# Optimization experiments

Measured on AMD Instinct MI355X. Metric: run time of the kernel, lower is better.

The kernel has to match this reference:

```python
import jax, jax.numpy as jnp
import numpy as np

DILATIONS = [1, 2, 4, 8, 16, 32, 64, 128, 256, 1, 2, 4, 8, 16, 32, 64, 128, 256]
KSIZE = 3
CHAN = 16
NUM_SIG = 1       # num_channels in original
NUM_CTRL = 3      # control channels appended to signal
FRAME_SIZE = 2048
R = sum(d * (KSIZE - 1) for d in DILATIONS) + 1  # 2045
BATCH = 64
T = FRAME_SIZE + R - 1  # 4092


def causal_conv1d(x, w, b, dil):
    # x: [B,T,Cin], w: [K,Cin,Cout] (Keras layout), causal left pad dil*(K-1)
    pad = dil * (w.shape[0] - 1)
    y = jax.lax.conv_general_dilated(
        x, w, window_strides=(1,), padding=[(pad, 0)],
        rhs_dilation=(dil,), dimension_numbers=("NWC", "WIO", "NWC"))
    return y + b


def setup_inputs() -> dict:
    key = jax.random.key(0)
    ks = jax.random.split(key, 8)
    n_layers = len(DILATIONS)
    in0 = NUM_SIG + NUM_CTRL            # layer 0 sees 1 signal + 3 controls = 4
    in_rest = CHAN + NUM_CTRL           # layers 1.. see 16-ch signal + 3 controls = 19
    s = 0.1
    inp = {
        "input": jax.random.normal(ks[0], (BATCH, T, in0), dtype=jnp.float32),
        "conv_w0": jax.random.normal(ks[1], (KSIZE, in0, CHAN), dtype=jnp.float32) * s,
        "conv_w": jax.random.normal(ks[2], (n_layers - 1, KSIZE, in_rest, CHAN), dtype=jnp.float32) * s,
        "conv_b": jax.random.normal(ks[3], (n_layers, CHAN), dtype=jnp.float32) * s,
        "io_w": jax.random.normal(ks[4], (n_layers - 1, CHAN, CHAN), dtype=jnp.float32) * s,
        "io_b": jax.random.normal(ks[5], (n_layers - 1, CHAN), dtype=jnp.float32) * s,
        "mixer_w": jax.random.normal(ks[6], (n_layers * CHAN, NUM_SIG), dtype=jnp.float32) * s,
        "mixer_b": jax.random.normal(ks[7], (NUM_SIG,), dtype=jnp.float32) * s,
    }
    return inp


def reference(input, conv_w0, conv_w, conv_b, io_w, io_b, mixer_w, mixer_b):
    signal = input[:, :, :NUM_SIG]        # [B,T,1]
    controls = input[:, :, NUM_SIG:]      # [B,T,3]
    n_layers = len(DILATIONS)
    acc = []
    for i in range(n_layers):
        w = conv_w0 if i == 0 else conv_w[i - 1]
        h = jnp.concatenate([signal, controls], axis=2)
        h = causal_conv1d(h, w, conv_b[i], DILATIONS[i])
        h = jax.nn.relu(h)                # [B,T,16]
        acc.append(h)
        if i != n_layers - 1:
            # 1x1 conv residual mix + halved channel-sum skip of previous signal
            signal = (jnp.einsum("btc,co->bto", h, io_w[i]) + io_b[i]
                      + jnp.sum(signal, axis=2, keepdims=True) / 2)
    accumulator = jnp.concatenate(acc, axis=2)  # [B,T,288]
    mixed = jnp.einsum("btc,co->bto", accumulator, mixer_w) + mixer_b
    return mixed[:, -FRAME_SIZE:, :]
```

## Files before the change

### kernel.cpp

```cpp
#include <hip/hip_runtime.h>

#define TFULL 4092
#define NB    64
#define CH    16
#define OUT_T 2048
#define TOFF  2044

__global__ __launch_bounds__(256) void layer0_kernel(
    const float* __restrict__ input,
    const float* __restrict__ w,
    const float* __restrict__ bias,
    const float* __restrict__ iow,
    const float* __restrict__ iob,
    const float* __restrict__ mw,
    const float* __restrict__ mb,
    float* __restrict__ sig_out,
    float* __restrict__ out)
{
    const int b = blockIdx.y;
    const int t = blockIdx.x * 256 + threadIdx.x;
    if (t >= TFULL) return;
    const float* ib = input + ((size_t)b * TFULL) * 4;

    float h[CH];
    #pragma unroll
    for (int o = 0; o < CH; ++o) h[o] = bias[o];

    float sig_t = 0.f;
    #pragma unroll
    for (int k = 0; k < 3; ++k) {
        const int tt = t - (2 - k);
        if (tt >= 0) {
            const float4 x = *(const float4*)(ib + (size_t)tt * 4);
            if (k == 2) sig_t = x.x;
            const float xv[4] = {x.x, x.y, x.z, x.w};
            #pragma unroll
            for (int c = 0; c < 4; ++c) {
                const float v = xv[c];
                #pragma unroll
                for (int o = 0; o < CH; ++o)
                    h[o] = fmaf(v, w[(k * 4 + c) * CH + o], h[o]);
            }
        }
    }
    #pragma unroll
    for (int o = 0; o < CH; ++o) h[o] = fmaxf(h[o], 0.f);

    if (t >= TOFF) {
        float m = mb[0];
        #pragma unroll
        for (int o = 0; o < CH; ++o) m = fmaf(h[o], mw[o], m);
        out[(size_t)b * OUT_T + (t - TOFF)] = m;
    }

    float sn[CH];
    const float half = sig_t * 0.5f;
    #pragma unroll
    for (int o = 0; o < CH; ++o) sn[o] = iob[o] + half;
    #pragma unroll
    for (int c = 0; c < CH; ++c) {
        const float v = h[c];
        #pragma unroll
        for (int o = 0; o < CH; ++o)
            sn[o] = fmaf(v, iow[c * CH + o], sn[o]);
    }
    float* op = sig_out + ((size_t)b * TFULL + t) * CH;
    *(float4*)(op + 0)  = make_float4(sn[0],  sn[1],  sn[2],  sn[3]);
    *(float4*)(op + 4)  = make_float4(sn[4],  sn[5],  sn[6],  sn[7]);
    *(float4*)(op + 8)  = make_float4(sn[8],  sn[9],  sn[10], sn[11]);
    *(float4*)(op + 12) = make_float4(sn[12], sn[13], sn[14], sn[15]);
}

template <bool HAS_IO>
__global__ __launch_bounds__(256) void layer_kernel(
    const float* __restrict__ input,
    const float* __restrict__ sig_in,
    const float* __restrict__ w,
    const float* __restrict__ bias,
    const float* __restrict__ iow,
    const float* __restrict__ iob,
    const float* __restrict__ mw,
    float* __restrict__ sig_out,
    float* __restrict__ out,
    int dil, int t_start)
{
    const int b = blockIdx.y;
    const int t = t_start + blockIdx.x * 256 + threadIdx.x;
    if (t >= TFULL) return;
    const float* ib = input  + ((size_t)b * TFULL) * 4;
    const float* sb = sig_in + ((size_t)b * TFULL) * CH;

    float h[CH];
    #pragma unroll
    for (int o = 0; o < CH; ++o) h[o] = bias[o];

    float sum_t = 0.f;
    #pragma unroll
    for (int k = 0; k < 3; ++k) {
        const int tt = t - (2 - k) * dil;
        if (tt >= 0) {
            const float4* sp = (const float4*)(sb + (size_t)tt * CH);
            const float4 s0 = sp[0], s1 = sp[1], s2 = sp[2], s3 = sp[3];
            const float sv[CH] = {s0.x, s0.y, s0.z, s0.w, s1.x, s1.y, s1.z, s1.w,
                                  s2.x, s2.y, s2.z, s2.w, s3.x, s3.y, s3.z, s3.w};
            const float4 cc = *(const float4*)(ib + (size_t)tt * 4);
            if (k == 2) {
                float acc = 0.f;
                #pragma unroll
                for (int c = 0; c < CH; ++c) acc += sv[c];
                sum_t = acc;
            }
            #pragma unroll
            for (int c = 0; c < CH; ++c) {
                const float v = sv[c];
                #pragma unroll
                for (int o = 0; o < CH; ++o)
                    h[o] = fmaf(v, w[(k * 19 + c) * CH + o], h[o]);
            }
            const float cv[3] = {cc.y, cc.z, cc.w};
            #pragma unroll
            for (int c = 0; c < 3; ++c) {
                const float v = cv[c];
                #pragma unroll
                for (int o = 0; o < CH; ++o)
                    h[o] = fmaf(v, w[(k * 19 + 16 + c) * CH + o], h[o]);
            }
        }
    }
    #pragma unroll
    for (int o = 0; o < CH; ++o) h[o] = fmaxf(h[o], 0.f);

    if (t >= TOFF) {
        float m = 0.f;
        #pragma unroll
        for (int o = 0; o < CH; ++o) m = fmaf(h[o], mw[o], m);
        const size_t oi = (size_t)b * OUT_T + (t - TOFF);
        out[oi] += m;
    }

    if (HAS_IO) {
        float sn[CH];
        const float half = sum_t * 0.5f;
        #pragma unroll
        for (int o = 0; o < CH; ++o) sn[o] = iob[o] + half;
        #pragma unroll
        for (int c = 0; c < CH; ++c) {
            const float v = h[c];
            #pragma unroll
            for (int o = 0; o < CH; ++o)
                sn[o] = fmaf(v, iow[c * CH + o], sn[o]);
        }
        float* op = sig_out + ((size_t)b * TFULL + t) * CH;
        *(float4*)(op + 0)  = make_float4(sn[0],  sn[1],  sn[2],  sn[3]);
        *(float4*)(op + 4)  = make_float4(sn[4],  sn[5],  sn[6],  sn[7]);
        *(float4*)(op + 8)  = make_float4(sn[8],  sn[9],  sn[10], sn[11]);
        *(float4*)(op + 12) = make_float4(sn[12], sn[13], sn[14], sn[15]);
    }
}

extern "C" void kernel_launch(void* const* d_in, const int* in_sizes, int n_in,
                              void* d_out, int out_size, void* d_ws, size_t ws_size,
                              hipStream_t stream) {
    const float* input   = (const float*)d_in[0];
    const float* conv_w0 = (const float*)d_in[1];
    const float* conv_w  = (const float*)d_in[2];
    const float* conv_b  = (const float*)d_in[3];
    const float* io_w    = (const float*)d_in[4];
    const float* io_b    = (const float*)d_in[5];
    const float* mixer_w = (const float*)d_in[6];
    const float* mixer_b = (const float*)d_in[7];
    float* out = (float*)d_out;

    float* sigA = (float*)d_ws;
    float* sigB = sigA + (size_t)NB * TFULL * CH;

    static const int dil[18] = {1,2,4,8,16,32,64,128,256, 1,2,4,8,16,32,64,128,256};
    static const int ts[18]  = {0,2,6,14,30,62,126,254,510,
                                1022,1024,1028,1036,1052,1084,1148,1276,1532};
    static const int ts17 = 2044;

    {
        dim3 grid((TFULL + 255) / 256, NB);
        layer0_kernel<<<grid, 256, 0, stream>>>(input, conv_w0, conv_b, io_w, io_b,
                                                mixer_w, mixer_b, sigA, out);
    }
    const float* cur = sigA;
    float* nxt = sigB;
    for (int i = 1; i < 18; ++i) {
        const int t0 = (i == 17) ? ts17 : ts[i];
        const int len = TFULL - t0;
        dim3 grid((len + 255) / 256, NB);
        const float* wl = conv_w + (size_t)(i - 1) * 3 * 19 * 16;
        if (i < 17) {
            layer_kernel<true><<<grid, 256, 0, stream>>>(
                input, cur, wl, conv_b + i * CH,
                io_w + (size_t)i * CH * CH, io_b + (size_t)i * CH,
                mixer_w + i * CH, nxt, out, dil[i], t0);
        } else {
            layer_kernel<false><<<grid, 256, 0, stream>>>(
                input, cur, wl, conv_b + i * CH,
                nullptr, nullptr,
                mixer_w + i * CH, nullptr, out, dil[i], t0);
        }
        float* tmp = (float*)cur; cur = nxt; nxt = tmp;
    }
}
```

Baseline: 323.8 us.

## Fuse dilated conv layers into three grouped kernels with shared-memory halo tiles

```diff
diff --git a/kernel.cpp b/kernel.cpp
--- a/kernel.cpp
+++ b/kernel.cpp
@@ -5,156 +5,179 @@
 #define CH    16
 #define OUT_T 2048
 #define TOFF  2044
-
-__global__ __launch_bounds__(256) void layer0_kernel(
+#define NT    512
+#define RSTRIDE 20
+
+template<int L0, int NL, int TILE, int HALO, bool FIRSTG, bool LASTG>
+__global__ __launch_bounds__(NT, 2) void group_kernel(
     const float* __restrict__ input,
-    const float* __restrict__ w,
-    const float* __restrict__ bias,
-    const float* __restrict__ iow,
-    const float* __restrict__ iob,
-    const float* __restrict__ mw,
-    const float* __restrict__ mb,
+    const float* __restrict__ conv_w0,
+    const float* __restrict__ conv_w,
+    const float* __restrict__ conv_b,
+    const float* __restrict__ io_w,
+    const float* __restrict__ io_b,
+    const float* __restrict__ mixer_w,
+    const float* __restrict__ mixer_b,
+    const float* __restrict__ sig_in,
     float* __restrict__ sig_out,
-    float* __restrict__ out)
+    float* __restrict__ out,
+    int out_start)
 {
-    const int b = blockIdx.y;
-    const int t = blockIdx.x * 256 + threadIdx.x;
-    if (t >= TFULL) return;
-    const float* ib = input + ((size_t)b * TFULL) * 4;
-
-    float h[CH];
-    #pragma unroll
-    for (int o = 0; o < CH; ++o) h[o] = bias[o];
-
-    float sig_t = 0.f;
-    #pragma unroll
-    for (int k = 0; k < 3; ++k) {
-        const int tt = t - (2 - k);
-        if (tt >= 0) {
-            const float4 x = *(const float4*)(ib + (size_t)tt * 4);
-            if (k == 2) sig_t = x.x;
-            const float xv[4] = {x.x, x.y, x.z, x.w};
-            #pragma unroll
-            for (int c = 0; c < 4; ++c) {
-                const float v = xv[c];
-                #pragma unroll
-                for (int o = 0; o < CH; ++o)
-                    h[o] = fmaf(v, w[(k * 4 + c) * CH + o], h[o]);
+    constexpr int NROWS = TILE + HALO;
+    __shared__ float buf[NROWS * RSTRIDE];
+    __shared__ float macc[TILE];
+
+    const int b       = blockIdx.y;
+    const int tile_lo = out_start + blockIdx.x * TILE;
+    const int tile_hi = (tile_lo + TILE < TFULL) ? (tile_lo + TILE) : TFULL;
+    const int buf_lo  = tile_lo - HALO;
+    const int tid     = threadIdx.x;
+
+    {
+        const float* ib = input + ((size_t)b * TFULL + buf_lo) * 4;
+        const int nstage = tile_hi - buf_lo;
+        for (int j = tid; j < nstage; j += NT) {
+            *(float4*)(&buf[j * RSTRIDE + 16]) = *(const float4*)(ib + (size_t)j * 4);
+            if constexpr (!FIRSTG) {
+                const float* sp = sig_in + ((size_t)b * TFULL + (buf_lo + j)) * CH;
+                *(float4*)(&buf[j * RSTRIDE + 0])  = *(const float4*)(sp + 0);
+                *(float4*)(&buf[j * RSTRIDE + 4])  = *(const float4*)(sp + 4);
+                *(float4*)(&buf[j * RSTRIDE + 8])  = *(const float4*)(sp + 8);
+                *(float4*)(&buf[j * RSTRIDE + 12]) = *(const float4*)(sp + 12);
             }
         }
+        for (int j = tid; j < TILE; j += NT) macc[j] = 0.f;
     }
-    #pragma unroll
-    for (int o = 0; o < CH; ++o) h[o] = fmaxf(h[o], 0.f);
-
-    if (t >= TOFF) {
-        float m = mb[0];
-        #pragma unroll
-        for (int o = 0; o < CH; ++o) m = fmaf(h[o], mw[o], m);
-        out[(size_t)b * OUT_T + (t - TOFF)] = m;
-    }
-
-    float sn[CH];
-    const float half = sig_t * 0.5f;
-    #pragma unroll
-    for (int o = 0; o < CH; ++o) sn[o] = iob[o] + half;
-    #pragma unroll
-    for (int c = 0; c < CH; ++c) {
-        const float v = h[c];
-        #pragma unroll
-        for (int o = 0; o < CH; ++o)
-            sn[o] = fmaf(v, iow[c * CH + o], sn[o]);
-    }
-    float* op = sig_out + ((size_t)b * TFULL + t) * CH;
-    *(float4*)(op + 0)  = make_float4(sn[0],  sn[1],  sn[2],  sn[3]);
-    *(float4*)(op + 4)  = make_float4(sn[4],  sn[5],  sn[6],  sn[7]);
-    *(float4*)(op + 8)  = make_float4(sn[8],  sn[9],  sn[10], sn[11]);
-    *(float4*)(op + 12) = make_float4(sn[12], sn[13], sn[14], sn[15]);
-}
-
-template <bool HAS_IO>
-__global__ __launch_bounds__(256) void layer_kernel(
-    const float* __restrict__ input,
-    const float* __restrict__ sig_in,
-    const float* __restrict__ w,
-    const float* __restrict__ bias,
-    const float* __restrict__ iow,
-    const float* __restrict__ iob,
-    const float* __restrict__ mw,
-    float* __restrict__ sig_out,
-    float* __restrict__ out,
-    int dil, int t_start)
-{
-    const int b = blockIdx.y;
-    const int t = t_start + blockIdx.x * 256 + threadIdx.x;
-    if (t >= TFULL) return;
-    const float* ib = input  + ((size_t)b * TFULL) * 4;
-    const float* sb = sig_in + ((size_t)b * TFULL) * CH;
-
-    float h[CH];
-    #pragma unroll
-    for (int o = 0; o < CH; ++o) h[o] = bias[o];
-
-    float sum_t = 0.f;
-    #pragma unroll
-    for (int k = 0; k < 3; ++k) {
-        const int tt = t - (2 - k) * dil;
-        if (tt >= 0) {
-            const float4* sp = (const float4*)(sb + (size_t)tt * CH);
-            const float4 s0 = sp[0], s1 = sp[1], s2 = sp[2], s3 = sp[3];
-            const float sv[CH] = {s0.x, s0.y, s0.z, s0.w, s1.x, s1.y, s1.z, s1.w,
-                                  s2.x, s2.y, s2.z, s2.w, s3.x, s3.y, s3.z, s3.w};
-            const float4 cc = *(const float4*)(ib + (size_t)tt * 4);
-            if (k == 2) {
-                float acc = 0.f;
+    __syncthreads();
+
+    int lo = buf_lo;
+    for (int i = 0; i < NL; ++i) {
+        const int g   = L0 + i;
+        const int dil = 1 << (g % 9);
+        lo += 2 * dil;
+        const bool lastl = (i == NL - 1);
+        const float* wb   = (g == 0) ? conv_w0 : (conv_w + (size_t)(g - 1) * 3 * 19 * CH);
+        const float* bias = conv_b  + (size_t)g * CH;
+        const float* iw   = io_w    + (size_t)g * CH * CH;
+        const float* iob2 = io_b    + (size_t)g * CH;
+        const float* mw   = mixer_w + (size_t)g * CH;
+
+        const int n   = tile_hi - lo;
+        const int nch = (n + NT - 1) / NT;
+        for (int c = 0; c < nch; ++c) {
+            const int r   = tile_hi - (c + 1) * NT + tid;
+            const bool act = (r >= lo);
+            int j = 0;
+            float sn[CH];
+            if (act) {
+                j = r - buf_lo;
+                const float* r2 = &buf[j * RSTRIDE];
+                const float* r1 = &buf[(j - dil) * RSTRIDE];
+                const float* r0 = &buf[(j - 2 * dil) * RSTRIDE];
+
+                float h[CH];
                 #pragma unroll
-                for (int c = 0; c < CH; ++c) acc += sv[c];
-                sum_t = acc;
+                for (int o = 0; o < CH; ++o) h[o] = bias[o];
+                float sum_t;
+
+                if (FIRSTG && g == 0) {
+                    const float4 x0 = *(const float4*)(r0 + 16);
+                    const float4 x1 = *(const float4*)(r1 + 16);
+                    const float4 x2 = *(const float4*)(r2 + 16);
+                    const float t0[4] = {x0.x, x0.y, x0.z, x0.w};
+                    const float t1[4] = {x1.x, x1.y, x1.z, x1.w};
+                    const float t2[4] = {x2.x, x2.y, x2.z, x2.w};
+                    #pragma unroll
+                    for (int cc = 0; cc < 4; ++cc) {
+                        #pragma unroll
+                        for (int o = 0; o < CH; ++o) {
+                            h[o] = fmaf(t0[cc], wb[(0 * 4 + cc) * CH + o], h[o]);
+                            h[o] = fmaf(t1[cc], wb[(1 * 4 + cc) * CH + o], h[o]);
+                            h[o] = fmaf(t2[cc], wb[(2 * 4 + cc) * CH + o], h[o]);
+                        }
+                    }
+                    sum_t = x2.x;
+                } else {
+                    const float4 a0 = *(const float4*)(r0 + 0),  a1 = *(const float4*)(r0 + 4),
+                                 a2 = *(const float4*)(r0 + 8),  a3 = *(const float4*)(r0 + 12),
+                                 a4 = *(const float4*)(r0 + 16);
+                    const float4 b0 = *(const float4*)(r1 + 0),  b1 = *(const float4*)(r1 + 4),
+                                 b2 = *(const float4*)(r1 + 8),  b3 = *(const float4*)(r1 + 12),
+                                 b4 = *(const float4*)(r1 + 16);
+                    const float4 c0 = *(const float4*)(r2 + 0),  c1 = *(const float4*)(r2 + 4),
+                                 c2 = *(const float4*)(r2 + 8),  c3 = *(const float4*)(r2 + 12),
+                                 c4 = *(const float4*)(r2 + 16);
+                    const float t0[19] = {a0.x,a0.y,a0.z,a0.w, a1.x,a1.y,a1.z,a1.w,
+                                          a2.x,a2.y,a2.z,a2.w, a3.x,a3.y,a3.z,a3.w,
+                                          a4.y,a4.z,a4.w};
+                    const float t1[19] = {b0.x,b0.y,b0.z,b0.w, b1.x,b1.y,b1.z,b1.w,
+                                          b2.x,b2.y,b2.z,b2.w, b3.x,b3.y,b3.z,b3.w,
+                                          b4.y,b4.z,b4.w};
+                    const float t2[19] = {c0.x,c0.y,c0.z,c0.w, c1.x,c1.y,c1.z,c1.w,
+                                          c2.x,c2.y,c2.z,c2.w, c3.x,c3.y,c3.z,c3.w,
+                                          c4.y,c4.z,c4.w};
+                    #pragma unroll
+                    for (int cc = 0; cc < 19; ++cc) {
+                        #pragma unroll
+                        for (int o = 0; o < CH; ++o) {
+                            h[o] = fmaf(t0[cc], wb[(0 * 19 + cc) * CH + o], h[o]);
+                            h[o] = fmaf(t1[cc], wb[(1 * 19 + cc) * CH + o], h[o]);
+                            h[o] = fmaf(t2[cc], wb[(2 * 19 + cc) * CH + o], h[o]);
+                        }
+                    }
+                    sum_t = ((c0.x + c0.y) + (c0.z + c0.w)) + ((c1.x + c1.y) + (c1.z + c1.w))
+                          + ((c2.x + c2.y) + (c2.z + c2.w)) + ((c3.x + c3.y) + (c3.z + c3.w));
+                }
+                #pragma unroll
+                for (int o = 0; o < CH; ++o) h[o] = fmaxf(h[o], 0.f);
+
+                if (r >= tile_lo && r >= TOFF) {
+                    float m = 0.f;
+                    #pragma unroll
+                    for (int o = 0; o < CH; ++o) m = fmaf(h[o], mw[o], m);
+                    macc[r - tile_lo] += m;
+                }
+
+                if (!(LASTG && lastl)) {
+                    const float half = 0.5f * sum_t;
+                    #pragma unroll
+                    for (int o = 0; o < CH; ++o) sn[o] = iob2[o] + half;
+                    #pragma unroll
+                    for (int cc = 0; cc < CH; ++cc) {
+                        #pragma unroll
+                        for (int o = 0; o < CH; ++o)
+                            sn[o] = fmaf(h[cc], iw[cc * CH + o], sn[o]);
+                    }
+                }
             }
-            #pragma unroll
-            for (int c = 0; c < CH; ++c) {
-                const float v = sv[c];
-                #pragma unroll
-                for (int o = 0; o < CH; ++o)
-                    h[o] = fmaf(v, w[(k * 19 + c) * CH + o], h[o]);
-            }
-            const float cv[3] = {cc.y, cc.z, cc.w};
-            #pragma unroll
-            for (int c = 0; c < 3; ++c) {
-                const float v = cv[c];
-                #pragma unroll
-                for (int o = 0; o < CH; ++o)
-                    h[o] = fmaf(v, w[(k * 19 + 16 + c) * CH + o], h[o]);
+            __syncthreads();
+            if (act) {
+                if (!lastl) {
+                    float* wp = &buf[j * RSTRIDE];
+                    *(float4*)(wp + 0)  = make_float4(sn[0],  sn[1],  sn[2],  sn[3]);
+                    *(float4*)(wp + 4)  = make_float4(sn[4],  sn[5],  sn[6],  sn[7]);
+                    *(float4*)(wp + 8)  = make_float4(sn[8],  sn[9],  sn[10], sn[11]);
+                    *(float4*)(wp + 12) = make_float4(sn[12], sn[13], sn[14], sn[15]);
+                } else if (!LASTG) {
+                    float* gp = sig_out + ((size_t)b * TFULL + r) * CH;
+                    *(float4*)(gp + 0)  = make_float4(sn[0],  sn[1],  sn[2],  sn[3]);
+                    *(float4*)(gp + 4)  = make_float4(sn[4],  sn[5],  sn[6],  sn[7]);
+                    *(float4*)(gp + 8)  = make_float4(sn[8],  sn[9],  sn[10], sn[11]);
+                    *(float4*)(gp + 12) = make_float4(sn[12], sn[13], sn[14], sn[15]);
+                }
             }
         }
+        __syncthreads();
     }
-    #pragma unroll
-    for (int o = 0; o < CH; ++o) h[o] = fmaxf(h[o], 0.f);
-
-    if (t >= TOFF) {
-        float m = 0.f;
-        #pragma unroll
-        for (int o = 0; o < CH; ++o) m = fmaf(h[o], mw[o], m);
-        const size_t oi = (size_t)b * OUT_T + (t - TOFF);
-        out[oi] += m;
-    }
-
-    if (HAS_IO) {
-        float sn[CH];
-        const float half = sum_t * 0.5f;
-        #pragma unroll
-        for (int o = 0; o < CH; ++o) sn[o] = iob[o] + half;
-        #pragma unroll
-        for (int c = 0; c < CH; ++c) {
-            const float v = h[c];
-            #pragma unroll
-            for (int o = 0; o < CH; ++o)
-                sn[o] = fmaf(v, iow[c * CH + o], sn[o]);
+
+    const int nmain = tile_hi - tile_lo;
+    for (int j = tid; j < nmain; j += NT) {
+        const int r = tile_lo + j;
+        if (r >= TOFF) {
+            const size_t oi = (size_t)b * OUT_T + (r - TOFF);
+            if (FIRSTG) out[oi] = mixer_b[0] + macc[j];
+            else        out[oi] += macc[j];
         }
-        float* op = sig_out + ((size_t)b * TFULL + t) * CH;
-        *(float4*)(op + 0)  = make_float4(sn[0],  sn[1],  sn[2],  sn[3]);
-        *(float4*)(op + 4)  = make_float4(sn[4],  sn[5],  sn[6],  sn[7]);
-        *(float4*)(op + 8)  = make_float4(sn[8],  sn[9],  sn[10], sn[11]);
-        *(float4*)(op + 12) = make_float4(sn[12], sn[13], sn[14], sn[15]);
     }
 }
 
@@ -174,34 +197,14 @@
     float* sigA = (float*)d_ws;
     float* sigB = sigA + (size_t)NB * TFULL * CH;
 
-    static const int dil[18] = {1,2,4,8,16,32,64,128,256, 1,2,4,8,16,32,64,128,256};
-    static const int ts[18]  = {0,2,6,14,30,62,126,254,510,
-                                1022,1024,1028,1036,1052,1084,1148,1276,1532};
-    static const int ts17 = 2044;
-
-    {
-        dim3 grid((TFULL + 255) / 256, NB);
-        layer0_kernel<<<grid, 256, 0, stream>>>(input, conv_w0, conv_b, io_w, io_b,
-                                                mixer_w, mixer_b, sigA, out);
-    }
-    const float* cur = sigA;
-    float* nxt = sigB;
-    for (int i = 1; i < 18; ++i) {
-        const int t0 = (i == 17) ? ts17 : ts[i];
-        const int len = TFULL - t0;
-        dim3 grid((len + 255) / 256, NB);
-        const float* wl = conv_w + (size_t)(i - 1) * 3 * 19 * 16;
-        if (i < 17) {
-            layer_kernel<true><<<grid, 256, 0, stream>>>(
-                input, cur, wl, conv_b + i * CH,
-                io_w + (size_t)i * CH * CH, io_b + (size_t)i * CH,
-                mixer_w + i * CH, nxt, out, dil[i], t0);
-        } else {
-            layer_kernel<false><<<grid, 256, 0, stream>>>(
-                input, cur, wl, conv_b + i * CH,
-                nullptr, nullptr,
-                mixer_w + i * CH, nullptr, out, dil[i], t0);
-        }
-        float* tmp = (float*)cur; cur = nxt; nxt = tmp;
-    }
+    dim3 block(NT, 1, 1);
+    group_kernel<0, 7, 1024, 254, true, false><<<dim3(4, NB), block, 0, stream>>>(
+        input, conv_w0, conv_w, conv_b, io_w, io_b, mixer_w, mixer_b,
+        nullptr, sigA, out, 254);
+    group_kernel<7, 6, 768, 798, false, false><<<dim3(4, NB), block, 0, stream>>>(
+        input, conv_w0, conv_w, conv_b, io_w, io_b, mixer_w, mixer_b,
+        sigA, sigB, out, 1052);
+    group_kernel<13, 5, 512, 992, false, true><<<dim3(4, NB), block, 0, stream>>>(
+        input, conv_w0, conv_w, conv_b, io_w, io_b, mixer_w, mixer_b,
+        sigB, nullptr, out, 2044);
 }
```

Result: slower. 431.0 us (+33.1%).
